# Performance work log

Measured on AMD Instinct MI355X. Metric: run time of the kernel, lower is better.

Reference implementation:

```python
import jax, jax.numpy as jnp
import numpy as np

B, CIN, L = 4, 128, 2048
D_MODEL, D_STATE, EXPAND, HEADDIM, NGROUPS = 256, 16, 3, 3, 1
D_INNER = EXPAND * D_MODEL            # 768
NHEADS = D_INNER // HEADDIM           # 256
CONV_DIM = D_INNER + 2 * NGROUPS * D_STATE   # 800
D_IN_PROJ = 2 * D_INNER + 2 * NGROUPS * D_STATE + NHEADS  # 1824
K_PROJ, D_CONV = 4, 4
EPS = 1e-5


def setup_inputs() -> dict:
    key = jax.random.key(0)
    ks = jax.random.split(key, 9)
    x = jax.random.normal(ks[0], (B, CIN, L), jnp.float32)
    proj_w = jax.random.normal(ks[1], (D_MODEL, CIN, K_PROJ), jnp.float32) / np.float32(np.sqrt(CIN * K_PROJ))
    in_proj_w = jax.random.normal(ks[2], (D_IN_PROJ, D_MODEL), jnp.float32) / np.float32(np.sqrt(D_MODEL))
    conv_w = jax.random.normal(ks[3], (CONV_DIM, 1, D_CONV), jnp.float32) / np.float32(np.sqrt(D_CONV))
    conv_b = jax.random.normal(ks[4], (CONV_DIM,), jnp.float32) * 0.01
    # dt_bias = inverse-softplus of dt ~ LogUniform[1e-3, 1e-1] (mamba2 init)
    u = jax.random.uniform(ks[5], (NHEADS,), jnp.float32)
    dt = jnp.exp(u * np.float32(np.log(0.1) - np.log(1e-3)) + np.float32(np.log(1e-3)))
    dt_bias = dt + jnp.log(-jnp.expm1(-dt))
    A_log = jnp.log(1.0 + 15.0 * jax.random.uniform(ks[6], (NHEADS,), jnp.float32))  # A in [-16,-1]
    D_skip = jnp.ones((NHEADS,), jnp.float32)
    norm_w = jnp.ones((D_INNER,), jnp.float32)
    out_proj_w = jax.random.normal(ks[7], (D_MODEL, D_INNER), jnp.float32) / np.float32(np.sqrt(D_INNER))
    return {"x": x, "proj_w": proj_w, "in_proj_w": in_proj_w, "conv_w": conv_w,
            "conv_b": conv_b, "dt_bias": dt_bias, "A_log": A_log, "D_skip": D_skip,
            "norm_w": norm_w, "out_proj_w": out_proj_w}


def _forward(x, proj_w, in_proj_w, conv_w, conv_b, dt_bias, A_log, D_skip, norm_w, out_proj_w):
    # outer Conv1d, padding='same' (k=4 -> left 1, right 2), no bias: (B,CIN,L)->(B,D_MODEL,L)
    h = jax.lax.conv_general_dilated(x, proj_w, (1,), [(1, 2)],
                                     dimension_numbers=("NCH", "OIH", "NCH"))
    u = h.transpose(0, 2, 1)                          # (B, L, d_model)
    zxbcdt = jnp.einsum("bld,ed->ble", u, in_proj_w)  # (B, L, 1824)
    z = zxbcdt[..., :D_INNER]                                     # (B,L,768)
    xBC = zxbcdt[..., D_INNER:D_INNER + CONV_DIM]                 # (B,L,800)
    dt = zxbcdt[..., D_INNER + CONV_DIM:]                         # (B,L,256)
    dt = jax.nn.softplus(dt + dt_bias)
    # depthwise causal conv (pad d_conv-1 on left) + SiLU
    xBC_c = jax.lax.conv_general_dilated(xBC.transpose(0, 2, 1), conv_w, (1,), [(D_CONV - 1, 0)],
                                         feature_group_count=CONV_DIM,
                                         dimension_numbers=("NCH", "OIH", "NCH"))
    xBC = jax.nn.silu(xBC_c + conv_b[None, :, None]).transpose(0, 2, 1)  # (B,L,800)
    xs = xBC[..., :D_INNER].reshape(B, L, NHEADS, HEADDIM)        # (B,L,H,P)
    Bm = xBC[..., D_INNER:D_INNER + D_STATE]                      # (B,L,N) (ngroups=1)
    Cm = xBC[..., D_INNER + D_STATE:]                             # (B,L,N)
    A = -jnp.exp(A_log)                                           # (H,)

    def step(hst, inp):
        dt_t, x_t, B_t, C_t = inp                 # (B,H),(B,H,P),(B,N),(B,N)
        dA = jnp.exp(dt_t * A)[:, :, None, None]  # (B,H,1,1)
        hst = dA * hst + jnp.einsum("bh,bhp,bn->bhpn", dt_t, x_t, B_t)
        y_t = jnp.einsum("bhpn,bn->bhp", hst, C_t)
        return hst, y_t

    h0 = jnp.zeros((B, NHEADS, HEADDIM, D_STATE), x.dtype)
    _, ys = jax.lax.scan(step, h0, (dt.transpose(1, 0, 2), xs.transpose(1, 0, 2, 3),
                                    Bm.transpose(1, 0, 2), Cm.transpose(1, 0, 2)))
    y = ys.transpose(1, 0, 2, 3) + D_skip[None, None, :, None] * xs   # (B,L,H,P)
    y = y.reshape(B, L, D_INNER)
    # gated RMSNorm: gate first, then normalize (norm_before_gate=False)
    y = y * jax.nn.silu(z)
    y = y * jax.lax.rsqrt(jnp.mean(y * y, axis=-1, keepdims=True) + EPS) * norm_w
    out = jnp.einsum("ble,de->bld", y, out_proj_w)   # (B,L,d_model)
    return out.transpose(0, 2, 1)                    # (B,d_model,L)


def reference(x, proj_w, in_proj_w, conv_w, conv_b, dt_bias, A_log, D_skip, norm_w, out_proj_w):
    return _forward(x, proj_w, in_proj_w, conv_w, conv_b, dt_bias, A_log, D_skip, norm_w, out_proj_w)
```

## Files before the change

kernel.cpp:

```cpp
#include <hip/hip_runtime.h>
#include <hip/hip_fp16.h>
#include <math.h>

#define B_     4
#define CIN    128
#define LEN    2048
#define DMODEL 256
#define DSTATE 16
#define NHEADS 256
#define DINNER 768
#define CONVDIM 800
#define DINPROJ 1824
#define EPS_   1e-5f
#define BAND   64
#define NBAND  32

typedef _Float16 f16x8 __attribute__((ext_vector_type(8)));
typedef _Float16 f16x4 __attribute__((ext_vector_type(4)));
typedef float    f32x4 __attribute__((ext_vector_type(4)));

__device__ __forceinline__ float silu_(float x){ return x / (1.0f + __expf(-x)); }
__device__ __forceinline__ float softplus_(float x){
    return x > 0.f ? x + log1pf(__expf(-x)) : log1pf(__expf(x));
}

__device__ __forceinline__ void gl2lds16(const _Float16* g, _Float16* l){
    __builtin_amdgcn_global_load_lds(
        (const __attribute__((address_space(1))) void*)g,
        (__attribute__((address_space(3))) void*)l, 16, 0, 0);
}

__global__ __launch_bounds__(256) void k_f2h(const float* __restrict__ a,
                                             _Float16* __restrict__ o, int n){
    for (int i = blockIdx.x * 256 + threadIdx.x; i < n; i += gridDim.x * 256)
        o[i] = (_Float16)a[i];
}

__global__ __launch_bounds__(256) void k_im2col(const float* __restrict__ x,
                                                _Float16* __restrict__ xcol){
    __shared__ float xs[CIN][68];
    int blk = blockIdx.x;
    int b  = blk >> 5;
    int l0 = (blk & 31) << 6;
    const float* xb = x + (size_t)b * CIN * LEN;
    for (int idx = threadIdx.x; idx < CIN * 67; idx += 256){
        int ci = idx / 67, j = idx % 67;
        int gl = l0 - 1 + j;
        xs[ci][j] = (gl >= 0 && gl < LEN) ? xb[ci * LEN + gl] : 0.f;
    }
    __syncthreads();
    #pragma unroll
    for (int v = 0; v < 16; v++){
        int id = v * 256 + threadIdx.x;
        int rl = id >> 6, c = id & 63;
        f16x8 pk;
        #pragma unroll
        for (int e = 0; e < 8; e++){
            int ci = c * 2 + (e >> 2), k = e & 3;
            pk[e] = (_Float16)xs[ci][rl + k];
        }
        *(f16x8*)&xcol[((size_t)(b * LEN + l0 + rl)) * 512 + c * 8] = pk;
    }
}

template<int K, int EPI>
__global__ __launch_bounds__(256) void k_gemm(const _Float16* __restrict__ A,
                                              const _Float16* __restrict__ Bw,
                                              const float* __restrict__ dt_bias,
                                              _Float16* __restrict__ o_u,
                                              _Float16* __restrict__ o_z,
                                              _Float16* __restrict__ o_xbc,
                                              _Float16* __restrict__ o_dt,
                                              float* __restrict__ o_f){
    __shared__ __align__(16) _Float16 As[128 * 32];
    __shared__ __align__(16) _Float16 Bs[128 * 32];
    __shared__ __align__(16) char EP[18432];
    int tid  = threadIdx.x;
    int wv   = tid >> 6;
    int lane = tid & 63;
    int quad = lane >> 4;
    int l16  = lane & 15;
    int m0 = blockIdx.x * 128;
    int n0 = blockIdx.y * 128;
    int wm = (wv >> 1) * 64;
    int wn = (wv & 1) * 64;
    int srow = lane >> 2;
    int scol = (lane & 3) * 8;

    f32x4 acc[4][4];
    #pragma unroll
    for (int i = 0; i < 4; i++)
        #pragma unroll
        for (int j = 0; j < 4; j++)
            acc[i][j] = (f32x4){0.f, 0.f, 0.f, 0.f};

    for (int k0 = 0; k0 < K; k0 += 32){
        #pragma unroll
        for (int j = 0; j < 2; j++){
            int ar = m0 + wv * 32 + j * 16 + srow;
            gl2lds16(A + (size_t)ar * K + k0 + scol,
                     &As[(wv * 32 + j * 16) * 32]);
            int nr = n0 + wv * 32 + j * 16 + srow;
            if (EPI == 1) nr = nr > (DINPROJ - 1) ? (DINPROJ - 1) : nr;
            gl2lds16(Bw + (size_t)nr * K + k0 + scol,
                     &Bs[(wv * 32 + j * 16) * 32]);
        }
        __syncthreads();
        f16x8 af[4], bf[4];
        #pragma unroll
        for (int i = 0; i < 4; i++)
            af[i] = *(const f16x8*)&As[(wm + i * 16 + l16) * 32 + quad * 8];
        #pragma unroll
        for (int j = 0; j < 4; j++)
            bf[j] = *(const f16x8*)&Bs[(wn + j * 16 + l16) * 32 + quad * 8];
        #pragma unroll
        for (int i = 0; i < 4; i++)
            #pragma unroll
            for (int j = 0; j < 4; j++)
                acc[i][j] = __builtin_amdgcn_mfma_f32_16x16x32_f16(
                                af[i], bf[j], acc[i][j], 0, 0, 0);
        __syncthreads();
    }

    if (EPI == 0 || EPI == 1){
        _Float16* T = (_Float16*)EP;
        #pragma unroll
        for (int p = 0; p < 2; p++){
            if (p) __syncthreads();
            {
                _Float16* Th = T + (wv >> 1) * (32 * 136);
                #pragma unroll
                for (int ii = 0; ii < 2; ii++){
                    int i = 2 * p + ii;
                    int r32 = i * 16 + quad * 4 - p * 32;
                    #pragma unroll
                    for (int j = 0; j < 4; j++){
                        int col = wn + j * 16 + l16;
                        #pragma unroll
                        for (int r = 0; r < 4; r++)
                            Th[(r32 + r) * 136 + col] = (_Float16)acc[i][j][r];
                    }
                }
            }
            __syncthreads();
            #pragma unroll
            for (int u = 0; u < 4; u++){
                int id = u * 256 + tid;
                int hb = id >> 9, rem = id & 511;
                int r32 = rem >> 4, cc = rem & 15;
                int grow = m0 + hb * 64 + p * 32 + r32;
                int abscol = n0 + cc * 8;
                f16x8 v = *(const f16x8*)&T[hb * (32 * 136) + r32 * 136 + cc * 8];
                if (EPI == 0){
                    *(f16x8*)&o_u[(size_t)grow * DMODEL + abscol] = v;
                } else {
                    if (abscol < DINNER){
                        *(f16x8*)&o_z[(size_t)grow * DINNER + abscol] = v;
                    } else if (abscol < DINNER + CONVDIM){
                        *(f16x8*)&o_xbc[(size_t)grow * CONVDIM + (abscol - DINNER)] = v;
                    } else if (abscol < DINPROJ){
                        int hh = abscol - (DINNER + CONVDIM);
                        f16x8 o;
                        #pragma unroll
                        for (int e = 0; e < 8; e++)
                            o[e] = (_Float16)softplus_((float)v[e] + dt_bias[hh + e]);
                        *(f16x8*)&o_dt[(size_t)grow * NHEADS + hh] = o;
                    }
                }
            }
        }
    } else {
        float* Tf = (float*)EP;
        int bb = m0 >> 11, ll0 = m0 & (LEN - 1);
        #pragma unroll
        for (int q = 0; q < 4; q++){
            if (q) __syncthreads();
            if ((wv >> 1) == (q >> 1)){
                #pragma unroll
                for (int ii = 0; ii < 2; ii++){
                    int i = (q & 1) * 2 + ii;
                    int r32 = i * 16 + quad * 4 - (q & 1) * 32;
                    #pragma unroll
                    for (int j = 0; j < 4; j++){
                        int col = wn + j * 16 + l16;
                        *(f32x4*)&Tf[col * 36 + r32] = acc[i][j];
                    }
                }
            }
            __syncthreads();
            #pragma unroll
            for (int u = 0; u < 4; u++){
                int id = u * 256 + tid;
                int col = id >> 3, seg = id & 7;
                f32x4 v = *(const f32x4*)&Tf[col * 36 + seg * 4];
                *(f32x4*)&o_f[(((size_t)(bb * DMODEL + n0 + col)) << 11)
                              + ll0 + q * 32 + seg * 4] = v;
            }
        }
    }
}

__global__ __launch_bounds__(256) void k_dwconv(const __half* __restrict__ xbc,
                                                const float* __restrict__ cw,
                                                const float* __restrict__ cb,
                                                __half* __restrict__ xcc){
    int idx = blockIdx.x * 256 + threadIdx.x;
    int c = idx % CONVDIM;
    int r = idx / CONVDIM;
    int l = r & (LEN - 1);
    float4 wv = *(const float4*)(cw + c * 4);
    float acc = cb[c];
    if (l >= 3){
        const __half* base = xbc + (size_t)(r - 3) * CONVDIM + c;
        acc += __half2float(base[0]) * wv.x + __half2float(base[CONVDIM]) * wv.y +
               __half2float(base[2 * CONVDIM]) * wv.z + __half2float(base[3 * CONVDIM]) * wv.w;
    } else {
        const float wk[4] = {wv.x, wv.y, wv.z, wv.w};
        for (int k = 0; k < 4; k++){
            int t = l - 3 + k;
            if (t >= 0) acc += __half2float(xbc[(size_t)(r + k - 3) * CONVDIM + c]) * wk[k];
        }
    }
    xcc[idx] = __float2half(silu_(acc));
}

__global__ __launch_bounds__(256) void k_y(const __half* __restrict__ dtb,
                                           const __half* __restrict__ xcc,
                                           const float* __restrict__ A_log,
                                           __half* __restrict__ y,
                                           float* __restrict__ E0,
                                           __half* __restrict__ cstate,
                                           float* __restrict__ dsum){
    __shared__ __align__(16) char smem[59392];
    __half* sBC = (__half*)smem;
    __half* sX  = (__half*)(smem + 4096);
    __half* sHL = (__half*)(smem + 4096);
    __half* sDT = (__half*)(smem + 28672);
    float*  sD  = (float*)(smem + 36864);
    float*  sG  = (float*)(smem + 54272);

    int band = blockIdx.x, hq = blockIdx.y, b = blockIdx.z;
    int row0 = band * BAND;
    int tid = threadIdx.x;
    int wv = tid >> 6, lane = tid & 63;

    {
        int c = wv, slot = c * 64 + lane;
        int row = slot >> 2, off = slot & 3;
        gl2lds16((const _Float16*)((const char*)xcc +
                   (size_t)(b * LEN + row0 + row) * 1600 + 1536 + off * 16),
                 (_Float16*)(smem + c * 1024));
    }
    #pragma unroll
    for (int i = 0; i < 6; i++){
        int c = wv + i * 4, slot = c * 64 + lane;
        int row = slot / 24, off = slot % 24;
        gl2lds16((const _Float16*)((const char*)xcc +
                   (size_t)(b * LEN + row0 + row) * 1600 + hq * 384 + off * 16),
                 (_Float16*)(smem + 4096 + c * 1024));
    }
    #pragma unroll
    for (int i = 0; i < 2; i++){
        int c = wv + i * 4, slot = c * 64 + lane;
        int row = slot >> 3, off = slot & 7;
        gl2lds16((const _Float16*)((const char*)dtb +
                   (size_t)(b * LEN + row0 + row) * 512 + hq * 128 + off * 16),
                 (_Float16*)(smem + 28672 + c * 1024));
    }
    __syncthreads();

    {
        int h = tid & 63, tb = tid >> 6;
        float A = -__expf(A_log[hq * 64 + h]);
        #pragma unroll
        for (int i = 0; i < 16; i++){
            int t = tb + i * 4;
            sD[t * 68 + h] = __expf(A * __half2float(sDT[t * 64 + h]));
        }
    }
    __syncthreads();

    if (tid < 64){
        int h = tid;
        float E = 1.f;
        float* ep = E0 + ((size_t)(b * LEN + row0)) * 256 + hq * 64 + h;
        for (int t = 0; t < 64; t++){
            E *= sD[t * 68 + h];
            *ep = E;
            ep += 256;
        }
        dsum[(size_t)(b * 256 + hq * 64 + h) * NBAND + band] = E;
    } else if (tid < 128){
        int tt = tid - 64;
        f16x8 ca = *(const f16x8*)&sBC[tt * 32 + 16];
        f16x8 cb = *(const f16x8*)&sBC[tt * 32 + 24];
        float cf[16];
        #pragma unroll
        for (int n = 0; n < 16; n++) cf[n] = (n < 8) ? (float)ca[n] : (float)cb[n - 8];
        for (int ss = 0; ss < 16; ss++){
            int s = (tt & 48) + ss;
            f16x8 ba = *(const f16x8*)&sBC[s * 32];
            f16x8 bb = *(const f16x8*)&sBC[s * 32 + 8];
            float acc = 0.f;
            #pragma unroll
            for (int n = 0; n < 8; n++)
                acc += cf[n] * (float)ba[n] + cf[n + 8] * (float)bb[n];
            sG[tt * 20 + ss] = acc;
        }
    } else {
        for (int idx = tid - 128; idx < 4096; idx += 128){
            int t = idx >> 6, h = idx & 63;
            float dtv = __half2float(sDT[t * 64 + h]);
            int xi = t * 192 + h * 3;
            sX[xi]     = __float2half(__half2float(sX[xi])     * dtv);
            sX[xi + 1] = __float2half(__half2float(sX[xi + 1]) * dtv);
            sX[xi + 2] = __float2half(__half2float(sX[xi + 2]) * dtv);
        }
    }
    __syncthreads();

    int t = tid >> 2, hsub = tid & 3, Hb = hsub * 16;
    int tmod = t & 15;
    float w[16], y0[16], y1[16], y2[16];
    #pragma unroll
    for (int i = 0; i < 16; i++){ w[i] = 1.f; y0[i] = 0.f; y1[i] = 0.f; y2[i] = 0.f; }

    for (int d = 0; d <= tmod; d++){
        int s = t - d;
        float g = sG[t * 20 + (tmod - d)];
        f32x4 Dv[4];
        #pragma unroll
        for (int k4 = 0; k4 < 4; k4++)
            Dv[k4] = *(const f32x4*)&sD[s * 68 + Hb + k4 * 4];
        f16x8 xv0 = *(const f16x8*)&sX[s * 192 + Hb * 3];
        f16x8 xv1 = *(const f16x8*)&sX[s * 192 + Hb * 3 + 8];
        f16x8 xv2 = *(const f16x8*)&sX[s * 192 + Hb * 3 + 16];
        f16x8 xv3 = *(const f16x8*)&sX[s * 192 + Hb * 3 + 24];
        f16x8 xv4 = *(const f16x8*)&sX[s * 192 + Hb * 3 + 32];
        f16x8 xv5 = *(const f16x8*)&sX[s * 192 + Hb * 3 + 40];
        #define XV(i) ((i)<8?(float)xv0[(i)]:(i)<16?(float)xv1[(i)-8]:(i)<24?(float)xv2[(i)-16]:\
                       (i)<32?(float)xv3[(i)-24]:(i)<40?(float)xv4[(i)-32]:(float)xv5[(i)-40])
        #pragma unroll
        for (int hh = 0; hh < 16; hh++){
            float wg = w[hh] * g;
            y0[hh] = fmaf(wg, XV(hh * 3 + 0), y0[hh]);
            y1[hh] = fmaf(wg, XV(hh * 3 + 1), y1[hh]);
            y2[hh] = fmaf(wg, XV(hh * 3 + 2), y2[hh]);
            w[hh] *= Dv[hh >> 2][hh & 3];
        }
        #undef XV
    }

    int h2 = tid >> 2, ng = tid & 3;
    float F[4][12];
    float vK[4];
    #pragma unroll
    for (int k = 0; k < 4; k++){
        #pragma unroll
        for (int i = 0; i < 12; i++) F[k][i] = 0.f;
        float v = 1.f;
        for (int ss = 15; ss >= 0; ss--){
            int s = k * 16 + ss;
            float x0 = __half2float(sX[s * 192 + h2 * 3]);
            float x1 = __half2float(sX[s * 192 + h2 * 3 + 1]);
            float x2 = __half2float(sX[s * 192 + h2 * 3 + 2]);
            f16x4 bv = *(const f16x4*)&sBC[s * 32 + ng * 4];
            #pragma unroll
            for (int nn = 0; nn < 4; nn++){
                float wb = v * (float)bv[nn];
                F[k][nn * 3 + 0] = fmaf(wb, x0, F[k][nn * 3 + 0]);
                F[k][nn * 3 + 1] = fmaf(wb, x1, F[k][nn * 3 + 1]);
                F[k][nn * 3 + 2] = fmaf(wb, x2, F[k][nn * 3 + 2]);
            }
            v *= sD[s * 68 + h2];
        }
        vK[k] = v;
    }

    __syncthreads();

    {
        float hc[12];
        #pragma unroll
        for (int i = 0; i < 12; i++) hc[i] = F[0][i];
        #pragma unroll
        for (int i = 0; i < 12; i++)
            sHL[(0 * 64 + h2) * 48 + ng * 12 + i] = __float2half(hc[i]);
        #pragma unroll
        for (int k = 1; k <= 2; k++){
            #pragma unroll
            for (int i = 0; i < 12; i++) hc[i] = fmaf(vK[k], hc[i], F[k][i]);
            #pragma unroll
            for (int i = 0; i < 12; i++)
                sHL[(k * 64 + h2) * 48 + ng * 12 + i] = __float2half(hc[i]);
        }
        __half* cp = cstate + ((size_t)((b * 256 + hq * 64 + h2) * NBAND + band)) * 48 + ng * 12;
        #pragma unroll
        for (int i = 0; i < 12; i++)
            cp[i] = __float2half(fmaf(vK[3], hc[i], F[3][i]));
    }
    __syncthreads();

    {
        f16x8 cva = *(const f16x8*)&sBC[t * 32 + 16];
        f16x8 cvb = *(const f16x8*)&sBC[t * 32 + 24];
        float cf[16];
        #pragma unroll
        for (int n = 0; n < 16; n++) cf[n] = (n < 8) ? (float)cva[n] : (float)cvb[n - 8];
        int k = t >> 4;
        if (k > 0){
            #pragma unroll
            for (int hh = 0; hh < 16; hh++){
                int h = Hb + hh;
                const __half* hl = &sHL[((k - 1) * 64 + h) * 48];
                f16x8 hv0 = *(const f16x8*)&hl[0];
                f16x8 hv1 = *(const f16x8*)&hl[8];
                f16x8 hv2 = *(const f16x8*)&hl[16];
                f16x8 hv3 = *(const f16x8*)&hl[24];
                f16x8 hv4 = *(const f16x8*)&hl[32];
                f16x8 hv5 = *(const f16x8*)&hl[40];
                #define HV(i) ((i)<8?(float)hv0[(i)]:(i)<16?(float)hv1[(i)-8]:(i)<24?(float)hv2[(i)-16]:\
                               (i)<32?(float)hv3[(i)-24]:(i)<40?(float)hv4[(i)-32]:(float)hv5[(i)-40])
                float a0 = 0.f, a1 = 0.f, a2 = 0.f;
                #pragma unroll
                for (int n = 0; n < 16; n++){
                    a0 = fmaf(cf[n], HV(n * 3 + 0), a0);
                    a1 = fmaf(cf[n], HV(n * 3 + 1), a1);
                    a2 = fmaf(cf[n], HV(n * 3 + 2), a2);
                }
                #undef HV
                y0[hh] = fmaf(w[hh], a0, y0[hh]);
                y1[hh] = fmaf(w[hh], a1, y1[hh]);
                y2[hh] = fmaf(w[hh], a2, y2[hh]);
            }
        }
        __half* yp = y + (size_t)(b * LEN + row0 + t) * DINNER + hq * 192 + hsub * 48;
        #pragma unroll
        for (int c = 0; c < 6; c++){
            f16x8 pk;
            #pragma unroll
            for (int e2 = 0; e2 < 8; e2++){
                int gi = c * 8 + e2;
                int hh = gi / 3, p = gi % 3;
                pk[e2] = (_Float16)(p == 0 ? y0[hh] : (p == 1 ? y1[hh] : y2[hh]));
            }
            *(f16x8*)&yp[c * 8] = pk;
        }
    }
}

__global__ __launch_bounds__(64) void k_scanB(__half* __restrict__ cstate,
                                              const float* __restrict__ dsum){
    int bh = blockIdx.x;
    int lane = threadIdx.x;
    if (lane >= 48) return;
    __half* st = cstate + (size_t)bh * NBAND * 48 + lane;
    const float* dd = dsum + (size_t)bh * NBAND;
    float H = 0.f;
    for (int c = 0; c < NBAND; c++){
        float d = dd[c];
        float s = __half2float(st[(size_t)c * 48]);
        st[(size_t)c * 48] = __float2half(H);
        H = fmaf(H, d, s);
    }
}

__global__ __launch_bounds__(256) void k_norm(__half* __restrict__ y,
                                              const __half* __restrict__ z,
                                              const __half* __restrict__ xcc,
                                              const float* __restrict__ E0,
                                              const __half* __restrict__ cstate,
                                              const float* __restrict__ D_skip,
                                              const float* __restrict__ nw){
    __shared__ __align__(16) char nsm[24576 + 64];
    __half* sHI = (__half*)nsm;
    float*  sCf = (float*)(nsm + 24576);
    __shared__ float wsum[4];
    int r = blockIdx.x;
    int b = r >> 11, l = r & (LEN - 1), band = l >> 6;
    int tid = threadIdx.x;
    int wv = tid >> 6, lane = tid & 63;

    #pragma unroll
    for (int i = 0; i < 6; i++){
        int chunk = (wv + i * 4) * 64 + lane;
        int head = chunk / 6, off = chunk % 6;
        gl2lds16((const _Float16*)((const char*)cstate +
                   ((size_t)(b * 256 + head) * NBAND + band) * 96 + off * 16),
                 (_Float16*)(nsm + (wv + i * 4) * 1024));
    }
    if (tid < 16)
        sCf[tid] = __half2float(xcc[(size_t)r * CONVDIM + DINNER + DSTATE + tid]);
    __syncthreads();

    const __half* zr = z + (size_t)r * DINNER;
    const __half* xr = xcc + (size_t)r * CONVDIM;
    const float*  er = E0 + (size_t)r * 256;
    __half* yr = y + (size_t)r * DINNER;
    float tv[3];
    #pragma unroll
    for (int q = 0; q < 3; q++){
        int e = tid + q * 256;
        int h = e / 3, p = e - h * 3;
        float corr = 0.f;
        #pragma unroll
        for (int n = 0; n < 16; n++)
            corr = fmaf(sCf[n], __half2float(sHI[h * 48 + n * 3 + p]), corr);
        float yf = __half2float(yr[e]) + er[h] * corr + D_skip[h] * __half2float(xr[e]);
        tv[q] = yf * silu_(__half2float(zr[e]));
    }
    float ss = tv[0] * tv[0] + tv[1] * tv[1] + tv[2] * tv[2];
    #pragma unroll
    for (int m = 1; m < 64; m <<= 1) ss += __shfl_xor(ss, m, 64);
    if ((tid & 63) == 0) wsum[tid >> 6] = ss;
    __syncthreads();
    float tot = wsum[0] + wsum[1] + wsum[2] + wsum[3];
    float sc = rsqrtf(tot / (float)DINNER + EPS_);
    #pragma unroll
    for (int q = 0; q < 3; q++){
        int e = tid + q * 256;
        yr[e] = __float2half(tv[q] * sc * nw[e]);
    }
}

extern "C" void kernel_launch(void* const* d_in, const int* in_sizes, int n_in,
                              void* d_out, int out_size, void* d_ws, size_t ws_size,
                              hipStream_t stream) {
    const float* x          = (const float*)d_in[0];
    const float* proj_w     = (const float*)d_in[1];
    const float* in_proj_w  = (const float*)d_in[2];
    const float* conv_w     = (const float*)d_in[3];
    const float* conv_b     = (const float*)d_in[4];
    const float* dt_bias    = (const float*)d_in[5];
    const float* A_log      = (const float*)d_in[6];
    const float* D_skip     = (const float*)d_in[7];
    const float* norm_w     = (const float*)d_in[8];
    const float* out_proj_w = (const float*)d_in[9];
    float* out = (float*)d_out;

    char* ob = (char*)d_out;
    _Float16* pw_h  = (_Float16*)ob;
    _Float16* ipw_h = (_Float16*)(ob + 262144);
    float*    E0    = (float*)d_out;

    char* wsb = (char*)d_ws;
    _Float16* xcol  = (_Float16*)(wsb);
    _Float16* u_h   = (_Float16*)(wsb + 8388608);
    __half*   xcc_h = (__half*)(wsb);
    __half*   z_h   = (__half*)(wsb + 13107200);
    __half*   xbc_h = (__half*)(wsb + 25690112);
    __half*   y_h   = xbc_h;
    __half*   dt_h  = (__half*)(wsb + 38797312);
    __half*   cstate= (__half*)(wsb + 42991616);
    float*    dsum  = (float*)(wsb + 46137344);
    _Float16* opw_h = (_Float16*)(wsb + 46268416);

    k_f2h   <<<64, 256, 0, stream>>>(proj_w,     pw_h,  DMODEL * CIN * 4);
    k_f2h   <<<64, 256, 0, stream>>>(in_proj_w,  ipw_h, DINPROJ * DMODEL);
    k_f2h   <<<64, 256, 0, stream>>>(out_proj_w, opw_h, DMODEL * DINNER);
    k_im2col<<<128, 256, 0, stream>>>(x, xcol);
    k_gemm<512, 0><<<dim3(64, 2), 256, 0, stream>>>(xcol, pw_h, nullptr,
        u_h, nullptr, nullptr, nullptr, nullptr);
    k_gemm<256, 1><<<dim3(64, 15), 256, 0, stream>>>(u_h, ipw_h, dt_bias,
        nullptr, (_Float16*)z_h, (_Float16*)xbc_h, (_Float16*)dt_h, nullptr);
    k_dwconv<<<25600, 256, 0, stream>>>(xbc_h, conv_w, conv_b, xcc_h);
    k_y     <<<dim3(NBAND, 4, B_), 256, 0, stream>>>(dt_h, xcc_h, A_log,
                                                     y_h, E0, cstate, dsum);
    k_scanB <<<1024, 64, 0, stream>>>(cstate, dsum);
    k_norm  <<<8192, 256, 0, stream>>>(y_h, z_h, xcc_h, E0, cstate,
                                       D_skip, norm_w);
    k_gemm<768, 2><<<dim3(64, 2), 256, 0, stream>>>((const _Float16*)y_h, opw_h,
        nullptr, nullptr, nullptr, nullptr, nullptr, out);
}
```

Before: 293.3 us.

## Double GEMM K-step with XOR-swizzled LDS tiles and merge weight-cast kernels

The GEMM main loop now loads 64-wide K slices per iteration instead of 32, so there are half as many barrier pairs. The LDS tiles use an XOR swizzle on the 16-byte column chunks, which is meant to avoid bank conflicts on the fragment reads. The A/B tiles and the epilogue buffer now share a single 32KB shared allocation, so LDS use does not grow. Separately, the three weight fp32-to-fp16 cast launches are merged into one kernel to cut launch overhead.

```diff
diff --git a/kernel.cpp b/kernel.cpp
--- a/kernel.cpp
+++ b/kernel.cpp
@@ -30,10 +30,19 @@
         (__attribute__((address_space(3))) void*)l, 16, 0, 0);
 }
 
-__global__ __launch_bounds__(256) void k_f2h(const float* __restrict__ a,
-                                             _Float16* __restrict__ o, int n){
-    for (int i = blockIdx.x * 256 + threadIdx.x; i < n; i += gridDim.x * 256)
-        o[i] = (_Float16)a[i];
+__global__ __launch_bounds__(256) void k_f2h3(const float* __restrict__ a0,
+                                              _Float16* __restrict__ o0, int n0,
+                                              const float* __restrict__ a1,
+                                              _Float16* __restrict__ o1, int n1,
+                                              const float* __restrict__ a2,
+                                              _Float16* __restrict__ o2, int n2){
+    int stride = gridDim.x * 256;
+    for (int i = blockIdx.x * 256 + threadIdx.x; i < n0; i += stride)
+        o0[i] = (_Float16)a0[i];
+    for (int i = blockIdx.x * 256 + threadIdx.x; i < n1; i += stride)
+        o1[i] = (_Float16)a1[i];
+    for (int i = blockIdx.x * 256 + threadIdx.x; i < n2; i += stride)
+        o2[i] = (_Float16)a2[i];
 }
 
 __global__ __launch_bounds__(256) void k_im2col(const float* __restrict__ x,
@@ -72,9 +81,10 @@
                                               _Float16* __restrict__ o_xbc,
                                               _Float16* __restrict__ o_dt,
                                               float* __restrict__ o_f){
-    __shared__ __align__(16) _Float16 As[128 * 32];
-    __shared__ __align__(16) _Float16 Bs[128 * 32];
-    __shared__ __align__(16) char EP[18432];
+    __shared__ __align__(16) char smem[32768];
+    _Float16* As = (_Float16*)smem;
+    _Float16* Bs = (_Float16*)(smem + 16384);
+    char* EP = smem;
     int tid  = threadIdx.x;
     int wv   = tid >> 6;
     int lane = tid & 63;
@@ -84,8 +94,6 @@
     int n0 = blockIdx.y * 128;
     int wm = (wv >> 1) * 64;
     int wn = (wv & 1) * 64;
-    int srow = lane >> 2;
-    int scol = (lane & 3) * 8;
 
     f32x4 acc[4][4];
     #pragma unroll
@@ -94,31 +102,38 @@
         for (int j = 0; j < 4; j++)
             acc[i][j] = (f32x4){0.f, 0.f, 0.f, 0.f};
 
-    for (int k0 = 0; k0 < K; k0 += 32){
-        #pragma unroll
-        for (int j = 0; j < 2; j++){
-            int ar = m0 + wv * 32 + j * 16 + srow;
-            gl2lds16(A + (size_t)ar * K + k0 + scol,
-                     &As[(wv * 32 + j * 16) * 32]);
-            int nr = n0 + wv * 32 + j * 16 + srow;
+    for (int k0 = 0; k0 < K; k0 += 64){
+        #pragma unroll
+        for (int j = 0; j < 4; j++){
+            int rbase = wv * 32 + j * 8;
+            int rrow  = rbase + (lane >> 3);
+            int cgl   = (lane & 7) ^ (lane >> 3);
+            int ar = m0 + rrow;
+            gl2lds16(A + (size_t)ar * K + k0 + cgl * 8, &As[rbase * 64]);
+            int nr = n0 + rrow;
             if (EPI == 1) nr = nr > (DINPROJ - 1) ? (DINPROJ - 1) : nr;
-            gl2lds16(Bw + (size_t)nr * K + k0 + scol,
-                     &Bs[(wv * 32 + j * 16) * 32]);
+            gl2lds16(Bw + (size_t)nr * K + k0 + cgl * 8, &Bs[rbase * 64]);
         }
         __syncthreads();
-        f16x8 af[4], bf[4];
-        #pragma unroll
-        for (int i = 0; i < 4; i++)
-            af[i] = *(const f16x8*)&As[(wm + i * 16 + l16) * 32 + quad * 8];
-        #pragma unroll
-        for (int j = 0; j < 4; j++)
-            bf[j] = *(const f16x8*)&Bs[(wn + j * 16 + l16) * 32 + quad * 8];
-        #pragma unroll
-        for (int i = 0; i < 4; i++)
+        #pragma unroll
+        for (int kk = 0; kk < 2; kk++){
+            f16x8 af[4], bf[4];
+            int sw = (l16 & 7);
+            #pragma unroll
+            for (int i = 0; i < 4; i++)
+                af[i] = *(const f16x8*)&As[(wm + i * 16 + l16) * 64 +
+                                           (((kk * 4 + quad) ^ sw) * 8)];
             #pragma unroll
             for (int j = 0; j < 4; j++)
-                acc[i][j] = __builtin_amdgcn_mfma_f32_16x16x32_f16(
-                                af[i], bf[j], acc[i][j], 0, 0, 0);
+                bf[j] = *(const f16x8*)&Bs[(wn + j * 16 + l16) * 64 +
+                                           (((kk * 4 + quad) ^ sw) * 8)];
+            #pragma unroll
+            for (int i = 0; i < 4; i++)
+                #pragma unroll
+                for (int j = 0; j < 4; j++)
+                    acc[i][j] = __builtin_amdgcn_mfma_f32_16x16x32_f16(
+                                    af[i], bf[j], acc[i][j], 0, 0, 0);
+        }
         __syncthreads();
     }
 
@@ -555,9 +570,9 @@
     float*    dsum  = (float*)(wsb + 46137344);
     _Float16* opw_h = (_Float16*)(wsb + 46268416);
 
-    k_f2h   <<<64, 256, 0, stream>>>(proj_w,     pw_h,  DMODEL * CIN * 4);
-    k_f2h   <<<64, 256, 0, stream>>>(in_proj_w,  ipw_h, DINPROJ * DMODEL);
-    k_f2h   <<<64, 256, 0, stream>>>(out_proj_w, opw_h, DMODEL * DINNER);
+    k_f2h3  <<<128, 256, 0, stream>>>(proj_w, pw_h, DMODEL * CIN * 4,
+                                      in_proj_w, ipw_h, DINPROJ * DMODEL,
+                                      out_proj_w, opw_h, DMODEL * DINNER);
     k_im2col<<<128, 256, 0, stream>>>(x, xcol);
     k_gemm<512, 0><<<dim3(64, 2), 256, 0, stream>>>(xcol, pw_h, nullptr,
         u_h, nullptr, nullptr, nullptr, nullptr);
```

Result: faster. 282.7 us (median of 3 runs) (-3.6%).
